# Performance work log

Hardware: AMD Instinct MI355X
Metric: run time of the kernel (lower is better)

Reference implementation:

```python
import jax, jax.numpy as jnp
import numpy as np

B, N, K = 8, 2048, 30
NF, EF = 128, 128
NPE, NRBF, MAXREL = 16, 16, 32


def _normalize(x, axis=-1, eps=1e-8):
    return x / (jnp.linalg.norm(x, axis=axis, keepdims=True) + eps)


def _gather_nodes(feat, idx):
    # feat [B,N,C], idx [B,N,K] -> [B,N,K,C]
    b = jnp.arange(feat.shape[0])[:, None, None]
    return feat[b, idx]


def _layernorm(x, g, b, eps=1e-5):
    mu = jnp.mean(x, -1, keepdims=True)
    var = jnp.var(x, -1, keepdims=True)
    return (x - mu) * jax.lax.rsqrt(var + eps) * g + b


def _dihedrals(X, eps=1e-7):
    # X [B,N,4,3]; use N,CA,C atoms -> [B,N,6] cos/sin of phi/psi/omega
    Bb, Nn = X.shape[0], X.shape[1]
    Xb = X[:, :, :3, :].reshape(Bb, 3 * Nn, 3)
    U = _normalize(Xb[:, 1:] - Xb[:, :-1])
    u2, u1, u0 = U[:, :-2], U[:, 1:-1], U[:, 2:]
    n2 = _normalize(jnp.cross(u2, u1))
    n1 = _normalize(jnp.cross(u1, u0))
    cosD = jnp.clip(jnp.sum(n2 * n1, -1), -1.0 + eps, 1.0 - eps)
    D = jnp.sign(jnp.sum(u2 * n1, -1)) * jnp.arccos(cosD)
    D = jnp.pad(D, ((0, 0), (1, 2))).reshape(Bb, Nn, 3)
    return jnp.concatenate([jnp.cos(D), jnp.sin(D)], -1)


def _quaternions(R):
    # R [B,N,K,3,3] -> unit quaternion [B,N,K,4]
    Rxx, Ryy, Rzz = R[..., 0, 0], R[..., 1, 1], R[..., 2, 2]
    mag = 0.5 * jnp.sqrt(jnp.abs(1.0 + jnp.stack(
        [Rxx - Ryy - Rzz, -Rxx + Ryy - Rzz, -Rxx - Ryy + Rzz], -1)))
    signs = jnp.sign(jnp.stack(
        [R[..., 2, 1] - R[..., 1, 2], R[..., 0, 2] - R[..., 2, 0], R[..., 1, 0] - R[..., 0, 1]], -1))
    xyz = signs * mag
    w = 0.5 * jnp.sqrt(jax.nn.relu(1.0 + Rxx + Ryy + Rzz))[..., None]
    return _normalize(jnp.concatenate([xyz, w], -1))


def _orientations_coarse(Ca, E_idx):
    # local backbone frames + neighbor direction (3) and relative quaternion (4)
    Bb, Nn = Ca.shape[0], Ca.shape[1]
    U = _normalize(Ca[:, 1:] - Ca[:, :-1])
    u2, u1 = U[:, :-2], U[:, 1:-1]
    n2 = _normalize(jnp.cross(u2, u1))
    o1 = _normalize(u2 - u1)
    O = jnp.stack([o1, n2, jnp.cross(o1, n2)], 2).reshape(Bb, Nn - 3, 9)
    O = jnp.pad(O, ((0, 0), (1, 2), (0, 0)))  # [B,N,9]
    O_nb = _gather_nodes(O, E_idx).reshape(Bb, Nn, -1, 3, 3)
    X_nb = _gather_nodes(Ca, E_idx)
    Of = O.reshape(Bb, Nn, 3, 3)
    dX = X_nb - Ca[:, :, None, :]
    dU = _normalize(jnp.einsum('bnij,bnkj->bnki', Of, dX))
    R = jnp.einsum('bnji,bnkjl->bnkil', Of, O_nb)  # O_i^T @ O_j
    Q = _quaternions(R)
    return jnp.concatenate([dU, Q], -1)  # [B,N,K,7]


def _rbf(D):
    mu = jnp.linspace(2.0, 22.0, NRBF)
    sigma = (22.0 - 2.0) / NRBF
    return jnp.exp(-(((D[..., None] - mu) / sigma) ** 2))


def setup_inputs() -> dict:
    key = jax.random.key(0)
    ks = jax.random.split(key, 8)
    X = jax.random.normal(ks[0], (B, N, 4, 3), dtype=jnp.float32)
    mask = jnp.ones((B, N), dtype=jnp.float32)
    residue_idx = jnp.arange(B * N, dtype=jnp.int32).reshape(B, N)
    chain_labels = jnp.zeros((B, N), dtype=jnp.int32)
    d_pe_in = 2 * MAXREL + 2  # 66
    e_in = NPE + NRBF + 7     # 39
    p = {
        'pe_w': jax.random.normal(ks[1], (d_pe_in, NPE)) / np.sqrt(d_pe_in),
        'pe_b': jnp.zeros((NPE,)),
        'node_l_w': jax.random.normal(ks[2], (6, NF)) / np.sqrt(6.0),
        'node_l_b': jnp.zeros((NF,)),
        'node_emb_w': jax.random.normal(ks[3], (NF, NF)) / np.sqrt(NF),
        'node_emb_b': jnp.zeros((NF,)),
        'edge_l_w': jax.random.normal(ks[4], (e_in, EF)) / np.sqrt(e_in),
        'edge_l_b': jnp.zeros((EF,)),
        'edge_emb_w': jax.random.normal(ks[5], (EF, EF)) / np.sqrt(EF),
        'edge_emb_b': jnp.zeros((EF,)),
        'nn_g': jnp.ones((NF,)), 'nn_b': jnp.zeros((NF,)),
        'ne_g': jnp.ones((EF,)), 'ne_b': jnp.zeros((EF,)),
    }
    return dict(X=X, mask=mask, residue_idx=residue_idx, chain_labels=chain_labels, **p)


def reference(X, mask, residue_idx, chain_labels, pe_w, pe_b, node_l_w, node_l_b,
              node_emb_w, node_emb_b, edge_l_w, edge_l_b, edge_emb_w, edge_emb_b,
              nn_g, nn_b, ne_g, ne_b):
    Ca = X[:, :, 1, :]
    mask2 = mask[:, :, None] * mask[:, None, :]
    D = jnp.sqrt(jnp.sum((Ca[:, :, None] - Ca[:, None, :]) ** 2, -1) + 1e-6)
    D_adj = D + (1.0 - mask2) * 10000.0
    negD, E_idx = jax.lax.top_k(-D_adj, K)  # k nearest
    D_nb = -negD                            # [B,N,K]
    RBF = _rbf(D_nb)                        # [B,N,K,16]
    O_feat = _orientations_coarse(Ca, E_idx)  # [B,N,K,7]
    # positional encodings on gathered residue offsets, masked by chain identity
    offset = residue_idx[:, :, None] - residue_idx[:, None, :]
    off_nb = jnp.take_along_axis(offset, E_idx, axis=2)
    chain_eq = (chain_labels[:, :, None] == chain_labels[:, None, :]).astype(jnp.int32)
    ch_nb = jnp.take_along_axis(chain_eq, E_idx, axis=2)
    d = jnp.clip(off_nb + MAXREL, 0, 2 * MAXREL) * ch_nb + (1 - ch_nb) * (2 * MAXREL + 1)
    d1h = jax.nn.one_hot(d, 2 * MAXREL + 2, dtype=jnp.float32)
    E_pos = d1h @ pe_w + pe_b               # [B,N,K,16]
    V = _dihedrals(X)                       # [B,N,6]
    E = jnp.concatenate([E_pos, RBF, O_feat], -1)  # [B,N,K,39]
    hV = (V @ node_l_w + node_l_b) @ node_emb_w + node_emb_b
    V_out = _layernorm(hV, nn_g, nn_b)
    hE = (E @ edge_l_w + edge_l_b) @ edge_emb_w + edge_emb_b
    E_out = _layernorm(hE, ne_g, ne_b)
    return V_out, E_out, E_idx
```

## Files before the change

kernel.cpp:

```cpp
#include <hip/hip_runtime.h>
#include <hip/hip_bf16.h>
#include <math.h>

#define BB 8
#define NN 2048
#define KK 30
#define NF 128
#define EF 128
#define NPE 16
#define NRBF 16
#define MAXREL 32

#define V_OUT_SZ   (BB*NN*NF)
#define E_OUT_OFF  (V_OUT_SZ)
#define E_OUT_SZ   (BB*NN*KK*EF)
#define EIDX_OUT_OFF (E_OUT_OFF + E_OUT_SZ)

#define WS_EIDX_OFF 0
#define WS_DNB_OFF  1966080
#define WS_O_OFF    3932160
#define WS_V6_OFF   4521984
#define WS_CA4_OFF  4915200
#define WS_W1_OFF   5177344
#define WS_W2_OFF   5193728

typedef __attribute__((ext_vector_type(8))) short bf16x8;
typedef __attribute__((ext_vector_type(4))) float f32x4;
#define MFMA16(a,b,c) __builtin_amdgcn_mfma_f32_16x16x32_bf16(a,b,c,0,0,0)

struct F3 { float x, y, z; };
__device__ inline F3 f3sub(F3 a, F3 b){ return {a.x-b.x, a.y-b.y, a.z-b.z}; }
__device__ inline F3 f3cross(F3 a, F3 b){ return {a.y*b.z - a.z*b.y, a.z*b.x - a.x*b.z, a.x*b.y - a.y*b.x}; }
__device__ inline float f3dot(F3 a, F3 b){ return a.x*b.x + a.y*b.y + a.z*b.z; }
__device__ inline F3 f3norm(F3 v){
    float n = sqrtf(f3dot(v, v));
    float r = 1.0f/(n + 1e-8f);
    return {v.x*r, v.y*r, v.z*r};
}
__device__ inline float sgnf(float x){ return (x>0.f)?1.f:((x<0.f)?-1.f:0.f); }
__device__ inline short f2bf(float f){
    union { __hip_bfloat16 h; short s; } u;
    u.h = __float2bfloat16(f);
    return u.s;
}

template<int CTRL>
__device__ __forceinline__ double kmin_dpp(double key){
    int hi = __double2hiint(key), lo = __double2loint(key);
    int ohi = __builtin_amdgcn_update_dpp(hi, hi, CTRL, 0xf, 0xf, false);
    int olo = __builtin_amdgcn_update_dpp(lo, lo, CTRL, 0xf, 0xf, false);
    return fmin(key, __hiloint2double(ohi, olo));
}

#if __has_builtin(__builtin_amdgcn_permlane16_swap)
__device__ __forceinline__ double kmin_x16(double key){
    unsigned hi = (unsigned)__double2hiint(key), lo = (unsigned)__double2loint(key);
    auto rh = __builtin_amdgcn_permlane16_swap(hi, hi, false, false);
    auto rl = __builtin_amdgcn_permlane16_swap(lo, lo, false, false);
    double a = __hiloint2double((int)rh[0], (int)rl[0]);
    double b = __hiloint2double((int)rh[1], (int)rl[1]);
    return fmin(key, fmin(a, b));
}
#else
__device__ __forceinline__ double kmin_x16(double key){
    int hi = __double2hiint(key), lo = __double2loint(key);
    int ohi = __builtin_amdgcn_ds_swizzle(hi, 0x401F);
    int olo = __builtin_amdgcn_ds_swizzle(lo, 0x401F);
    return fmin(key, __hiloint2double(ohi, olo));
}
#endif

#if __has_builtin(__builtin_amdgcn_permlane32_swap)
__device__ __forceinline__ double kmin_x32(double key){
    unsigned hi = (unsigned)__double2hiint(key), lo = (unsigned)__double2loint(key);
    auto rh = __builtin_amdgcn_permlane32_swap(hi, hi, false, false);
    auto rl = __builtin_amdgcn_permlane32_swap(lo, lo, false, false);
    double a = __hiloint2double((int)rh[0], (int)rl[0]);
    double b = __hiloint2double((int)rh[1], (int)rl[1]);
    return fmin(key, fmin(a, b));
}
#else
__device__ __forceinline__ double kmin_x32(double key){
    return fmin(key, __shfl_xor(key, 32, 64));
}
#endif

__device__ __forceinline__ double wave_min64(double k){
    k = kmin_dpp<0xB1>(k);
    k = kmin_dpp<0x4E>(k);
    k = kmin_dpp<0x124>(k);
    k = kmin_dpp<0x128>(k);
    k = kmin_x16(k);
    k = kmin_x32(k);
    return k;
}

__device__ __forceinline__ double half_min32(double k){
    k = kmin_dpp<0xB1>(k);
    k = kmin_dpp<0x4E>(k);
    k = kmin_dpp<0x124>(k);
    k = kmin_dpp<0x128>(k);
    k = kmin_x16(k);
    return k;
}

__global__ void prep_kernel(const float* __restrict__ elw,
                            const float* __restrict__ eew,
                            __hip_bfloat16* __restrict__ w1,
                            __hip_bfloat16* __restrict__ w2)
{
    int i = blockIdx.x*256 + threadIdx.x;
    if (i < 8192) {
        int j = i & 7, lane = (i>>3)&63, ks = (i>>9)&1, nf = i>>10;
        int k = ks*32 + (lane>>4)*8 + j;
        int col = nf*16 + (lane&15);
        float v = (k < 39) ? elw[k*128 + col] : 0.f;
        w1[i] = __float2bfloat16(v);
    } else if (i < 8192 + 16384) {
        int i2 = i - 8192;
        int j = i2 & 7, lane = (i2>>3)&63, ks = (i2>>9)&3, nf = i2>>11;
        int k = ks*32 + (lane>>4)*8 + j;
        int col = nf*16 + (lane&15);
        w2[i2] = __float2bfloat16(eew[k*128 + col]);
    }
}

__global__ void geom_kernel(const float* __restrict__ X,
                            const float* __restrict__ mask,
                            float* __restrict__ wsO, float* __restrict__ wsV6,
                            float4* __restrict__ wsCa4)
{
    int ng = blockIdx.x * blockDim.x + threadIdx.x;
    if (ng >= BB*NN) return;
    int b = ng / NN, n = ng % NN;
    const float* Xb = X + (size_t)b * NN * 12;

    {
        const float* cp = X + (size_t)ng*12 + 3;
        wsCa4[ng] = make_float4(cp[0], cp[1], cp[2], mask[ng]);
    }

    int k0 = 3*n - 1;
    F3 P[6];
    #pragma unroll
    for (int t = 0; t < 6; ++t) {
        int m = k0 + t;
        if (m < 0) m = 0;
        if (m > 3*NN-1) m = 3*NN-1;
        int r = m / 3, a = m % 3;
        const float* p = Xb + ((size_t)r*4 + a)*3;
        P[t] = {p[0], p[1], p[2]};
    }
    F3 U[5];
    #pragma unroll
    for (int t = 0; t < 5; ++t) U[t] = f3norm(f3sub(P[t+1], P[t]));

    float Dang[3];
    #pragma unroll
    for (int t = 0; t < 3; ++t) {
        int k = k0 + t;
        if (k < 0 || k > 3*NN-4) { Dang[t] = 0.f; continue; }
        F3 u2 = U[t], u1 = U[t+1], u0 = U[t+2];
        F3 n2 = f3norm(f3cross(u2, u1));
        F3 n1 = f3norm(f3cross(u1, u0));
        float cosD = f3dot(n2, n1);
        cosD = fminf(fmaxf(cosD, -1.f + 1e-7f), 1.f - 1e-7f);
        float s = f3dot(u2, n1);
        Dang[t] = sgnf(s) * acosf(cosD);
    }
    float* v6 = wsV6 + (size_t)ng * 6;
    v6[0] = cosf(Dang[0]); v6[1] = cosf(Dang[1]); v6[2] = cosf(Dang[2]);
    v6[3] = sinf(Dang[0]); v6[4] = sinf(Dang[1]); v6[5] = sinf(Dang[2]);

    float* o = wsO + (size_t)ng * 9;
    if (n >= 1 && n <= NN-3) {
        const float* cb = X + (size_t)b * NN * 12 + 3;
        F3 c0 = {cb[(size_t)(n-1)*12+0], cb[(size_t)(n-1)*12+1], cb[(size_t)(n-1)*12+2]};
        F3 c1 = {cb[(size_t)(n  )*12+0], cb[(size_t)(n  )*12+1], cb[(size_t)(n  )*12+2]};
        F3 c2 = {cb[(size_t)(n+1)*12+0], cb[(size_t)(n+1)*12+1], cb[(size_t)(n+1)*12+2]};
        F3 u2 = f3norm(f3sub(c1, c0));
        F3 u1 = f3norm(f3sub(c2, c1));
        F3 n2 = f3norm(f3cross(u2, u1));
        F3 o1 = f3norm(f3sub(u2, u1));
        F3 r2 = f3cross(o1, n2);
        o[0]=o1.x; o[1]=o1.y; o[2]=o1.z;
        o[3]=n2.x; o[4]=n2.y; o[5]=n2.z;
        o[6]=r2.x; o[7]=r2.y; o[8]=r2.z;
    } else {
        #pragma unroll
        for (int m = 0; m < 9; ++m) o[m] = 0.f;
    }
}

#define TOPK_SENT 1.0e300

__global__ __launch_bounds__(256) void topk_kernel(
    const float4* __restrict__ wsCa4,
    int* __restrict__ wsEidx, float* __restrict__ wsDnb,
    float* __restrict__ outEidxF)
{
    __shared__ float dist[4][NN];
    const int wave = threadIdx.x >> 6, lane = threadIdx.x & 63;
    const int row = blockIdx.x*4 + wave;
    const int b = row >> 11, i = row & (NN-1);
    float* dd = dist[wave];

    const float4* cb = wsCa4 + ((size_t)b << 11);
    float4 ci = cb[i];
    float mi = ci.w;

    double lmin = TOPK_SENT;
    #pragma unroll 8
    for (int s = 0; s < NN/64; ++s) {
        int j = s*64 + lane;
        float4 cj = cb[j];
        float dx = ci.x - cj.x, dy = ci.y - cj.y, dz = ci.z - cj.z;
        float d = sqrtf(dx*dx + dy*dy + dz*dz + 1e-6f);
        d += (1.0f - mi * cj.w) * 10000.0f;
        dd[s*64 + ((lane + s) & 63)] = d;
        unsigned long long key =
            ((unsigned long long)__float_as_uint(d) << 32) | (unsigned)j;
        lmin = fmin(lmin, __longlong_as_double((long long)key));
    }

    const size_t rb = (size_t)row * KK;
    for (int k = 0; k < KK; ++k) {
        double g = wave_min64(lmin);
        unsigned long long gk = (unsigned long long)__double_as_longlong(g);
        int j = (int)(unsigned)gk;
        float dwin = __uint_as_float((unsigned)(gk >> 32));
        if (lane == 0) {
            wsEidx[rb + k] = j;
            wsDnb[rb + k]  = dwin;
            outEidxF[rb + k] = (float)j;
        }
        const int wl = j & 63, wslot = j >> 6;

        if (lane == 0) dd[wslot*64 + ((wl + wslot) & 63)] = 3.402823466e+38f;

        int s = lane & 31;
        float dr = dd[s*64 + ((wl + s) & 63)];
        unsigned long long ck =
            ((unsigned long long)__float_as_uint(dr) << 32) | (unsigned)s;
        double c = half_min32(__longlong_as_double((long long)ck));
        unsigned long long ck0 = (unsigned long long)__double_as_longlong(c);
        unsigned s2 = (unsigned)ck0;
        unsigned long long nk =
            (ck0 & 0xFFFFFFFF00000000ULL) | (unsigned)(s2*64 + wl);
        if (lane == wl) lmin = __longlong_as_double((long long)nk);
    }
}

__global__ __launch_bounds__(128) void node_kernel(
    const float* __restrict__ wsV6,
    const float* __restrict__ nlw, const float* __restrict__ nlb,
    const float* __restrict__ new_, const float* __restrict__ neb,
    const float* __restrict__ nng, const float* __restrict__ nnb,
    float* __restrict__ outV)
{
    int f = threadIdx.x;
    __shared__ float h1[128];
    __shared__ float red[2][2];

    float w2[128];
    #pragma unroll
    for (int c = 0; c < 128; ++c) w2[c] = new_[c*128 + f];
    float w1[6];
    #pragma unroll
    for (int c = 0; c < 6; ++c) w1[c] = nlw[c*128 + f];
    float b1v = nlb[f], b2v = neb[f], gv = nng[f], bv = nnb[f];

    for (int gi = 0; gi < 8; ++gi) {
        int row = blockIdx.x*8 + gi;
        float acc = b1v;
        #pragma unroll
        for (int c = 0; c < 6; ++c) acc = fmaf(wsV6[(size_t)row*6 + c], w1[c], acc);
        h1[f] = acc;
        __syncthreads();

        float a2 = b2v;
        #pragma unroll
        for (int c4 = 0; c4 < 32; ++c4) {
            float4 v = *(const float4*)&h1[c4*4];
            a2 = fmaf(v.x, w2[c4*4+0], a2);
            a2 = fmaf(v.y, w2[c4*4+1], a2);
            a2 = fmaf(v.z, w2[c4*4+2], a2);
            a2 = fmaf(v.w, w2[c4*4+3], a2);
        }
        float s = a2, ss = a2*a2;
        #pragma unroll
        for (int off = 32; off; off >>= 1) {
            s  += __shfl_xor(s,  off, 64);
            ss += __shfl_xor(ss, off, 64);
        }
        int wig = f >> 6;
        if ((f & 63) == 0) { red[wig][0] = s; red[wig][1] = ss; }
        __syncthreads();
        float S = red[0][0] + red[1][0], SS = red[0][1] + red[1][1];
        float mu = S * (1.f/128.f);
        float var = SS * (1.f/128.f) - mu*mu;
        float inv = rsqrtf(var + 1e-5f);
        outV[(size_t)row*128 + f] = (a2 - mu)*inv*gv + bv;
        __syncthreads();
    }
}

__global__ __launch_bounds__(256, 4) void edge_mfma_kernel(
    const float4* __restrict__ wsCa4,
    const int* __restrict__ ridx, const int* __restrict__ chain,
    const int* __restrict__ wsEidx, const float* __restrict__ wsDnb,
    const float* __restrict__ wsO,
    const float* __restrict__ pe_w, const float* __restrict__ pe_b,
    const __hip_bfloat16* __restrict__ wsW1, const __hip_bfloat16* __restrict__ wsW2,
    const float* __restrict__ elb, const float* __restrict__ eeb,
    const float* __restrict__ lng, const float* __restrict__ lnb,
    float* __restrict__ outE)
{
    __shared__ char smem[64*72*2 + 64*136*2];
    short* Ef  = (short*)smem;
    short* h1t = (short*)(smem + 64*72*2);
    float* redS  = (float*)smem;
    float* redSS = (float*)(smem + 512);

    const int tid  = threadIdx.x;
    const int wave = tid >> 6, lane = tid & 63;
    const int wm = wave >> 1, wn = wave & 1;
    const int lr = lane & 15, lk = lane >> 4;

    float b1v[4], b2v[4], gv[4], bv[4];
    #pragma unroll
    for (int nf = 0; nf < 4; ++nf) {
        int col = wn*64 + nf*16 + lr;
        b1v[nf] = elb[col]; b2v[nf] = eeb[col];
        gv[nf]  = lng[col]; bv[nf]  = lnb[col];
    }

    for (int idx = tid; idx < 64*25; idx += 256) {
        int r = idx / 25, c = 39 + idx % 25;
        Ef[r*72 + c] = 0;
    }

    const int E0 = blockIdx.x * 64;

    if (wave == 0) {
        int ge = E0 + lane;
        int row = ge / KK;
        int b = row >> 11;
        int j = wsEidx[ge];
        float oi[9], oj[9];
        #pragma unroll
        for (int m = 0; m < 9; ++m) {
            oi[m] = wsO[(size_t)row*9 + m];
            oj[m] = wsO[((size_t)(b*NN) + j)*9 + m];
        }
        float4 ci = wsCa4[row];
        float4 cj = wsCa4[(size_t)b*NN + j];
        float dx = cj.x-ci.x, dy = cj.y-ci.y, dz = cj.z-ci.z;
        float t0 = oi[0]*dx + oi[1]*dy + oi[2]*dz;
        float t1 = oi[3]*dx + oi[4]*dy + oi[5]*dz;
        float t2 = oi[6]*dx + oi[7]*dy + oi[8]*dz;
        float nr = sqrtf(t0*t0 + t1*t1 + t2*t2);
        float iv = 1.f/(nr + 1e-8f);
        short* ef = &Ef[lane*72];
        ef[32] = f2bf(t0*iv); ef[33] = f2bf(t1*iv); ef[34] = f2bf(t2*iv);
        float R00 = oi[0]*oj[0]+oi[3]*oj[3]+oi[6]*oj[6];
        float R01 = oi[0]*oj[1]+oi[3]*oj[4]+oi[6]*oj[7];
        float R02 = oi[0]*oj[2]+oi[3]*oj[5]+oi[6]*oj[8];
        float R10 = oi[1]*oj[0]+oi[4]*oj[3]+oi[7]*oj[6];
        float R11 = oi[1]*oj[1]+oi[4]*oj[4]+oi[7]*oj[7];
        float R12 = oi[1]*oj[2]+oi[4]*oj[5]+oi[7]*oj[8];
        float R20 = oi[2]*oj[0]+oi[5]*oj[3]+oi[8]*oj[6];
        float R21 = oi[2]*oj[1]+oi[5]*oj[4]+oi[8]*oj[7];
        float R22 = oi[2]*oj[2]+oi[5]*oj[5]+oi[8]*oj[8];
        float mx = 0.5f*sqrtf(fabsf(1.f + R00 - R11 - R22));
        float my = 0.5f*sqrtf(fabsf(1.f - R00 + R11 - R22));
        float mz = 0.5f*sqrtf(fabsf(1.f - R00 - R11 + R22));
        float qx = sgnf(R21 - R12)*mx;
        float qy = sgnf(R02 - R20)*my;
        float qz = sgnf(R10 - R01)*mz;
        float qw = 0.5f*sqrtf(fmaxf(0.f, 1.f + R00 + R11 + R22));
        float qn = sqrtf(qx*qx + qy*qy + qz*qz + qw*qw);
        float qi = 1.f/(qn + 1e-8f);
        ef[35] = f2bf(qx*qi); ef[36] = f2bf(qy*qi);
        ef[37] = f2bf(qz*qi); ef[38] = f2bf(qw*qi);
    } else if (wave == 1) {
        int ge = E0 + lane;
        float dnb = wsDnb[ge];
        short* ef = &Ef[lane*72 + 16];
        #pragma unroll
        for (int m = 0; m < 16; ++m) {
            float mu = 2.f + (20.f/15.f)*(float)m;
            float z = (dnb - mu) * 0.8f;
            ef[m] = f2bf(expf(-z*z));
        }
    } else if (wave == 2) {
        int ge = E0 + lane;
        int row = ge / KK;
        int b = row >> 11;
        int j = wsEidx[ge];
        int ri = ridx[row], rj = ridx[b*NN + j];
        int ch = (chain[row] == chain[b*NN + j]) ? 1 : 0;
        int dd = min(max(ri - rj + MAXREL, 0), 2*MAXREL);
        dd = ch ? dd : (2*MAXREL + 1);
        short* ef = &Ef[lane*72];
        #pragma unroll
        for (int m = 0; m < 16; ++m) ef[m] = f2bf(pe_w[dd*16 + m] + pe_b[m]);
    }
    __syncthreads();

    const bf16x8* W1f = (const bf16x8*)wsW1;
    const bf16x8* W2f = (const bf16x8*)wsW2;

    f32x4 acc[2][4];
    #pragma unroll
    for (int mf = 0; mf < 2; ++mf)
        #pragma unroll
        for (int nf = 0; nf < 4; ++nf)
            acc[mf][nf] = (f32x4){0.f, 0.f, 0.f, 0.f};
    #pragma unroll
    for (int ks = 0; ks < 2; ++ks) {
        bf16x8 a0 = *(const bf16x8*)&Ef[(wm*32      + lr)*72 + ks*32 + lk*8];
        bf16x8 a1 = *(const bf16x8*)&Ef[(wm*32 + 16 + lr)*72 + ks*32 + lk*8];
        #pragma unroll
        for (int nf = 0; nf < 4; ++nf) {
            bf16x8 Bf = W1f[((wn*4 + nf)*2 + ks)*64 + lane];
            acc[0][nf] = MFMA16(a0, Bf, acc[0][nf]);
            acc[1][nf] = MFMA16(a1, Bf, acc[1][nf]);
        }
    }
    #pragma unroll
    for (int mf = 0; mf < 2; ++mf)
        #pragma unroll
        for (int nf = 0; nf < 4; ++nf)
            #pragma unroll
            for (int r = 0; r < 4; ++r) {
                int row = wm*32 + mf*16 + lk*4 + r;
                int col = wn*64 + nf*16 + lr;
                h1t[row*136 + col] = f2bf(acc[mf][nf][r] + b1v[nf]);
            }
    __syncthreads();

    f32x4 acc2[2][4];
    #pragma unroll
    for (int mf = 0; mf < 2; ++mf)
        #pragma unroll
        for (int nf = 0; nf < 4; ++nf)
            acc2[mf][nf] = (f32x4){0.f, 0.f, 0.f, 0.f};
    #pragma unroll
    for (int ks = 0; ks < 4; ++ks) {
        bf16x8 a0 = *(const bf16x8*)&h1t[(wm*32      + lr)*136 + ks*32 + lk*8];
        bf16x8 a1 = *(const bf16x8*)&h1t[(wm*32 + 16 + lr)*136 + ks*32 + lk*8];
        #pragma unroll
        for (int nf = 0; nf < 4; ++nf) {
            bf16x8 Bf = W2f[((wn*4 + nf)*4 + ks)*64 + lane];
            acc2[0][nf] = MFMA16(a0, Bf, acc2[0][nf]);
            acc2[1][nf] = MFMA16(a1, Bf, acc2[1][nf]);
        }
    }
    #pragma unroll
    for (int mf = 0; mf < 2; ++mf)
        #pragma unroll
        for (int nf = 0; nf < 4; ++nf)
            #pragma unroll
            for (int r = 0; r < 4; ++r)
                acc2[mf][nf][r] += b2v[nf];

    #pragma unroll
    for (int mf = 0; mf < 2; ++mf) {
        #pragma unroll
        for (int r = 0; r < 4; ++r) {
            float v0 = acc2[mf][0][r], v1 = acc2[mf][1][r];
            float v2 = acc2[mf][2][r], v3 = acc2[mf][3][r];
            float s = v0 + v1 + v2 + v3;
            float q = v0*v0 + v1*v1 + v2*v2 + v3*v3;
            #pragma unroll
            for (int off = 1; off < 16; off <<= 1) {
                s += __shfl_xor(s, off, 64);
                q += __shfl_xor(q, off, 64);
            }
            if (lr == 0) {
                int row = wm*32 + mf*16 + lk*4 + r;
                redS[row*2 + wn] = s; redSS[row*2 + wn] = q;
            }
        }
    }
    __syncthreads();

    const size_t obase = (size_t)E0 * 128;
    #pragma unroll
    for (int mf = 0; mf < 2; ++mf) {
        #pragma unroll
        for (int r = 0; r < 4; ++r) {
            int row = wm*32 + mf*16 + lk*4 + r;
            float S = redS[row*2 + 0] + redS[row*2 + 1];
            float Q = redSS[row*2 + 0] + redSS[row*2 + 1];
            float mu = S * (1.f/128.f);
            float var = Q * (1.f/128.f) - mu*mu;
            float inv = rsqrtf(var + 1e-5f);
            #pragma unroll
            for (int nf = 0; nf < 4; ++nf) {
                int col = wn*64 + nf*16 + lr;
                outE[obase + (size_t)row*128 + col] =
                    (acc2[mf][nf][r] - mu)*inv*gv[nf] + bv[nf];
            }
        }
    }
}

extern "C" void kernel_launch(void* const* d_in, const int* in_sizes, int n_in,
                              void* d_out, int out_size, void* d_ws, size_t ws_size,
                              hipStream_t stream)
{
    const float* X     = (const float*)d_in[0];
    const float* mask  = (const float*)d_in[1];
    const int*   ridx  = (const int*)  d_in[2];
    const int*   chain = (const int*)  d_in[3];
    const float* pe_w  = (const float*)d_in[4];
    const float* pe_b  = (const float*)d_in[5];
    const float* nlw   = (const float*)d_in[6];
    const float* nlb   = (const float*)d_in[7];
    const float* new_  = (const float*)d_in[8];
    const float* neb   = (const float*)d_in[9];
    const float* elw   = (const float*)d_in[10];
    const float* elb   = (const float*)d_in[11];
    const float* eew   = (const float*)d_in[12];
    const float* eeb   = (const float*)d_in[13];
    const float* nng   = (const float*)d_in[14];
    const float* nnb   = (const float*)d_in[15];
    const float* neg_  = (const float*)d_in[16];
    const float* neb_  = (const float*)d_in[17];

    float* out = (float*)d_out;
    char*  ws  = (char*)d_ws;
    int*    wsEidx = (int*)   (ws + WS_EIDX_OFF);
    float*  wsDnb  = (float*) (ws + WS_DNB_OFF);
    float*  wsO    = (float*) (ws + WS_O_OFF);
    float*  wsV6   = (float*) (ws + WS_V6_OFF);
    float4* wsCa4  = (float4*)(ws + WS_CA4_OFF);
    __hip_bfloat16* wsW1 = (__hip_bfloat16*)(ws + WS_W1_OFF);
    __hip_bfloat16* wsW2 = (__hip_bfloat16*)(ws + WS_W2_OFF);

    prep_kernel<<<96, 256, 0, stream>>>(elw, eew, wsW1, wsW2);
    geom_kernel<<<(BB*NN + 255)/256, 256, 0, stream>>>(X, mask, wsO, wsV6, wsCa4);
    topk_kernel<<<BB*NN/4, 256, 0, stream>>>(wsCa4, wsEidx, wsDnb, out + EIDX_OUT_OFF);
    node_kernel<<<BB*NN/8, 128, 0, stream>>>(wsV6, nlw, nlb, new_, neb, nng, nnb, out);
    edge_mfma_kernel<<<BB*NN*KK/64, 256, 0, stream>>>(wsCa4, ridx, chain, wsEidx, wsDnb, wsO,
                                                      pe_w, pe_b, wsW1, wsW2,
                                                      elb, eeb, neg_, neb_, out + E_OUT_OFF);
}
```

Baseline: 202.0 us.

## Replace shared-memory topk rescans with per-lane register top-3 queues

The top-k kernel no longer stores distances in shared memory. Each lane keeps its 32 distances in registers along with a sorted queue of its three smallest packed keys. Each of the 30 rounds does one wave-wide min, and only the winning lane pops its queue, refilling from registers when the queue runs empty. Results are buffered per lane and written once at the end, which removes the LDS traffic and the per-round half-wave reduction. The cost is higher register pressure and occasional divergent refill loops; explicit round-to-nearest float ops keep the distances bit-identical to the reference.

```diff
diff --git a/kernel.cpp b/kernel.cpp
--- a/kernel.cpp
+++ b/kernel.cpp
@@ -92,15 +92,6 @@
     k = kmin_dpp<0x128>(k);
     k = kmin_x16(k);
     k = kmin_x32(k);
-    return k;
-}
-
-__device__ __forceinline__ double half_min32(double k){
-    k = kmin_dpp<0xB1>(k);
-    k = kmin_dpp<0x4E>(k);
-    k = kmin_dpp<0x124>(k);
-    k = kmin_dpp<0x128>(k);
-    k = kmin_x16(k);
     return k;
 }
 
@@ -192,62 +183,77 @@
     }
 }
 
-#define TOPK_SENT 1.0e300
-
-__global__ __launch_bounds__(256) void topk_kernel(
+#define KEMPTY 8.9884656743115795e+307
+
+__device__ __forceinline__ double make_key(float d, int j){
+    unsigned long long k =
+        ((unsigned long long)__float_as_uint(d) << 32) | (unsigned)j;
+    return __longlong_as_double((long long)k);
+}
+
+__device__ __forceinline__ void ins3(double& q0, double& q1, double& q2, double k){
+    double k2 = fmin(k, q2);
+    double t1 = fmin(q1, k2); q2 = fmax(q1, k2);
+    double t0 = fmin(q0, t1); q1 = fmax(q0, t1);
+    q0 = t0;
+}
+
+__global__ __launch_bounds__(256, 4) void topk_kernel(
     const float4* __restrict__ wsCa4,
     int* __restrict__ wsEidx, float* __restrict__ wsDnb,
     float* __restrict__ outEidxF)
 {
-    __shared__ float dist[4][NN];
     const int wave = threadIdx.x >> 6, lane = threadIdx.x & 63;
     const int row = blockIdx.x*4 + wave;
     const int b = row >> 11, i = row & (NN-1);
-    float* dd = dist[wave];
 
     const float4* cb = wsCa4 + ((size_t)b << 11);
     float4 ci = cb[i];
     float mi = ci.w;
 
-    double lmin = TOPK_SENT;
+    float dloc[32];
+    double q0 = KEMPTY, q1 = KEMPTY, q2 = KEMPTY;
     #pragma unroll 8
-    for (int s = 0; s < NN/64; ++s) {
+    for (int s = 0; s < 32; ++s) {
         int j = s*64 + lane;
         float4 cj = cb[j];
-        float dx = ci.x - cj.x, dy = ci.y - cj.y, dz = ci.z - cj.z;
-        float d = sqrtf(dx*dx + dy*dy + dz*dz + 1e-6f);
-        d += (1.0f - mi * cj.w) * 10000.0f;
-        dd[s*64 + ((lane + s) & 63)] = d;
-        unsigned long long key =
-            ((unsigned long long)__float_as_uint(d) << 32) | (unsigned)j;
-        lmin = fmin(lmin, __longlong_as_double((long long)key));
-    }
-
-    const size_t rb = (size_t)row * KK;
+        float dx = __fsub_rn(ci.x, cj.x);
+        float dy = __fsub_rn(ci.y, cj.y);
+        float dz = __fsub_rn(ci.z, cj.z);
+        float d2 = __fadd_rn(__fadd_rn(__fadd_rn(__fmul_rn(dx,dx),
+                                                 __fmul_rn(dy,dy)),
+                                       __fmul_rn(dz,dz)), 1e-6f);
+        float d = sqrtf(d2);
+        d = __fadd_rn(d, __fmul_rn(__fsub_rn(1.0f, __fmul_rn(mi, cj.w)), 10000.0f));
+        dloc[s] = d;
+        ins3(q0, q1, q2, make_key(d, j));
+    }
+
+    double res = KEMPTY;
     for (int k = 0; k < KK; ++k) {
-        double g = wave_min64(lmin);
-        unsigned long long gk = (unsigned long long)__double_as_longlong(g);
+        double g = wave_min64(q0);
+        if (lane == k) res = g;
+        if (__double_as_longlong(q0) == __double_as_longlong(g)) {
+            q0 = q1; q1 = q2; q2 = KEMPTY;
+            if (__double_as_longlong(q0) == __double_as_longlong(KEMPTY)) {
+                #pragma unroll 4
+                for (int s = 0; s < 32; ++s) {
+                    double kk = make_key(dloc[s], s*64 + lane);
+                    if (!(kk > g)) kk = KEMPTY;
+                    ins3(q0, q1, q2, kk);
+                }
+            }
+        }
+    }
+
+    if (lane < KK) {
+        const size_t rb = (size_t)row * KK;
+        unsigned long long gk = (unsigned long long)__double_as_longlong(res);
         int j = (int)(unsigned)gk;
         float dwin = __uint_as_float((unsigned)(gk >> 32));
-        if (lane == 0) {
-            wsEidx[rb + k] = j;
-            wsDnb[rb + k]  = dwin;
-            outEidxF[rb + k] = (float)j;
-        }
-        const int wl = j & 63, wslot = j >> 6;
-
-        if (lane == 0) dd[wslot*64 + ((wl + wslot) & 63)] = 3.402823466e+38f;
-
-        int s = lane & 31;
-        float dr = dd[s*64 + ((wl + s) & 63)];
-        unsigned long long ck =
-            ((unsigned long long)__float_as_uint(dr) << 32) | (unsigned)s;
-        double c = half_min32(__longlong_as_double((long long)ck));
-        unsigned long long ck0 = (unsigned long long)__double_as_longlong(c);
-        unsigned s2 = (unsigned)ck0;
-        unsigned long long nk =
-            (ck0 & 0xFFFFFFFF00000000ULL) | (unsigned)(s2*64 + wl);
-        if (lane == wl) lmin = __longlong_as_double((long long)nk);
+        wsEidx[rb + lane] = j;
+        wsDnb[rb + lane]  = dwin;
+        outEidxF[rb + lane] = (float)j;
     }
 }
 
```

After: 187.7 us. -7.1%, faster.
